# Optimization experiments

Hardware: AMD Instinct MI355X
Metric: run time of the kernel (lower is better)

## Reference

```python
import jax, jax.numpy as jnp
import numpy as np

D_MODEL = 1024
N_STATE = 16
D_INNER = 2 * D_MODEL          # 2048
DT_RANK = (D_MODEL + 15) // 16  # 64 = ceil(d/16)
K_CONV = 4
B, L = 1, 1024


def setup_inputs() -> dict:
    key = jax.random.key(0)
    ks = jax.random.split(key, 9)
    s = lambda fan_in: 1.0 / np.sqrt(fan_in)
    x = jax.random.normal(ks[0], (B, L, D_MODEL), dtype=jnp.float32)
    W_in = jax.random.normal(ks[1], (D_MODEL, 2 * D_INNER), dtype=jnp.float32) * s(D_MODEL)
    conv_w = jax.random.normal(ks[2], (D_INNER, K_CONV), dtype=jnp.float32) * s(K_CONV)
    conv_b = jnp.zeros((D_INNER,), dtype=jnp.float32)
    W_x = jax.random.normal(ks[3], (D_INNER, DT_RANK + 2 * N_STATE), dtype=jnp.float32) * s(D_INNER)
    W_dt = jax.random.normal(ks[4], (DT_RANK, D_INNER), dtype=jnp.float32) * s(DT_RANK)
    b_dt = jax.random.normal(ks[5], (D_INNER,), dtype=jnp.float32) * 0.01
    # A_log initialized as log(1..N) repeated over d_inner, as in __init__
    A_log = jnp.log(jnp.broadcast_to(jnp.arange(1, N_STATE + 1, dtype=jnp.float32), (D_INNER, N_STATE)))
    D = jnp.ones((D_INNER,), dtype=jnp.float32)
    W_out = jax.random.normal(ks[6], (D_INNER, D_MODEL), dtype=jnp.float32) * s(D_INNER)
    return {"x": x, "W_in": W_in, "conv_w": conv_w, "conv_b": conv_b,
            "W_x": W_x, "W_dt": W_dt, "b_dt": b_dt, "A_log": A_log,
            "D": D, "W_out": W_out}


def _causal_dw_conv(x, w, b):
    # x: [B,L,C], w: [C,K], b: [C]; causal depthwise conv (pad left K-1)
    K = w.shape[1]
    xp = jnp.pad(x, ((0, 0), (K - 1, 0), (0, 0)))
    Lx = x.shape[1]
    out = b
    for k in range(K):  # small fixed K=4
        out = out + xp[:, k:k + Lx, :] * w[:, k]
    return out


def _selective_scan(u, delta, A, Bm, Cm, D):
    # u,delta: [B,L,Di]; A: [Di,N]; Bm,Cm: [B,L,N]; D: [Di]
    dA = jnp.exp(delta[..., None] * A)                      # [B,L,Di,N]
    dBu = delta[..., None] * Bm[:, :, None, :] * u[..., None]
    dA_t = jnp.moveaxis(dA, 1, 0)    # [L,B,Di,N]
    dBu_t = jnp.moveaxis(dBu, 1, 0)
    C_t = jnp.moveaxis(Cm, 1, 0)     # [L,B,N]

    def step(h, inp):
        dA_i, dBu_i, C_i = inp
        h = dA_i * h + dBu_i
        y = jnp.einsum('bdn,bn->bd', h, C_i)
        return h, y

    h0 = jnp.zeros(u.shape[:1] + A.shape, dtype=u.dtype)  # [B,Di,N]
    _, ys = jax.lax.scan(step, h0, (dA_t, dBu_t, C_t))
    y = jnp.moveaxis(ys, 0, 1)       # [B,L,Di]
    return y + u * D


def reference(x, W_in, conv_w, conv_b, W_x, W_dt, b_dt, A_log, D, W_out):
    silu = jax.nn.silu
    x_and_res = x @ W_in                                   # [B,L,2*Di]
    x_in, res = jnp.split(x_and_res, 2, axis=-1)
    x_conv = silu(_causal_dw_conv(x_in, conv_w, conv_b))   # [B,L,Di]
    x_dbl = x_conv @ W_x                                   # [B,L,dt_rank+2N]
    dt, Bm, Cm = jnp.split(x_dbl, [DT_RANK, DT_RANK + N_STATE], axis=-1)
    delta = jax.nn.softplus(dt @ W_dt + b_dt)              # [B,L,Di]
    A = -jnp.exp(A_log)                                    # [Di,N]
    y = _selective_scan(x_conv, delta, A, Bm, Cm, D)
    return (y * silu(res)) @ W_out                         # [B,L,d_model]
```

## Files before the change

### kernel.cpp

```cpp
#include <hip/hip_runtime.h>

typedef unsigned short u16;
typedef unsigned int u32;
typedef __attribute__((ext_vector_type(8))) short bf16x8;
typedef __attribute__((ext_vector_type(4))) float f32x4;

#define LSEQ 1024

__device__ __forceinline__ float b2f(u16 v) { return __uint_as_float(((u32)v) << 16); }
__device__ __forceinline__ u16 f2b(float f) {
    u32 x = __float_as_uint(f);
    return (u16)((x + 0x7fffu + ((x >> 16) & 1u)) >> 16);
}
__device__ __forceinline__ float rdf(const void* p, size_t i, int f) {
    return f ? b2f(((const u16*)p)[i]) : ((const float*)p)[i];
}
__device__ __forceinline__ float fsig(float x) {
    return __builtin_amdgcn_rcpf(1.f + __expf(-x));
}

typedef const __attribute__((address_space(1))) u32* gp_t;
typedef __attribute__((address_space(3))) u32* lp_t;
__device__ __forceinline__ void gload16(const u16* g, u16* lds_wave_base) {
    __builtin_amdgcn_global_load_lds((gp_t)g, (lp_t)lds_wave_base, 16, 0, 0);
}

__global__ __launch_bounds__(256) void prep_k(const void* __restrict__ x,
                                              const void* __restrict__ W_in,
                                              const void* __restrict__ W_out,
                                              const void* __restrict__ W_x,
                                              const void* __restrict__ W_dt,
                                              u16* __restrict__ xb,
                                              u16* __restrict__ W_in_t,
                                              u16* __restrict__ W_out_t,
                                              u16* __restrict__ W_x_t,
                                              u16* __restrict__ W_dt_t,
                                              int* __restrict__ flag) {
    __shared__ int cnt;
    __shared__ __align__(8) u16 tile[32][36];
    if (threadIdx.x == 0) cnt = 0;
    __syncthreads();
    const u16* xu = (const u16*)x;
    int c = 0;
#pragma unroll
    for (int j = 0; j < 8; ++j) {
        u16 u = xu[threadIdx.x * 8 + j];
        int e = (u >> 7) & 0xFF;
        c += (e == 0 || (e >= 100 && e <= 140)) ? 1 : 0;
    }
    atomicAdd(&cnt, c);
    __syncthreads();
    const int f = (cnt >= 1638) ? 1 : 0;
    if (blockIdx.x == 0 && threadIdx.x == 0) *flag = f;

    int blk = blockIdx.x;
    if (blk < 1024) {
        int i = (blk * 256 + threadIdx.x) * 4;
        ushort4 o;
        if (f) {
            o = *(const ushort4*)(xu + i);
        } else {
            float4 v = *(const float4*)((const float*)x + i);
            o = make_ushort4(f2b(v.x), f2b(v.y), f2b(v.z), f2b(v.w));
        }
        *(ushort4*)(xb + i) = o;
        return;
    }
    blk -= 1024;
    const void* src; u16* dst; int R, Cn, nbc, t;
    if (blk < 4096)      { src = W_in;  dst = W_in_t;  R = 1024; Cn = 4096; nbc = 128; t = blk; }
    else if (blk < 6144) { src = W_out; dst = W_out_t; R = 2048; Cn = 1024; nbc = 32;  t = blk - 4096; }
    else if (blk < 6400) { src = W_x;   dst = W_x_t;   R = 2048; Cn = 96;   nbc = 4;   t = blk - 6144; }
    else                 { src = W_dt;  dst = W_dt_t;  R = 64;   Cn = 2048; nbc = 64;  t = blk - 6400; }
    int br = t / nbc, bc = t - br * nbc;
    int r0 = br * 32, c0 = bc * 32;
    {
        int ty = threadIdx.x >> 3, tx4 = (threadIdx.x & 7) << 2;
        u16 o0 = 0, o1 = 0, o2 = 0, o3 = 0;
        if (c0 + tx4 < Cn) {
            size_t off = (size_t)(r0 + ty) * Cn + c0 + tx4;
            if (f) {
                ushort4 u = *(const ushort4*)((const u16*)src + off);
                o0 = u.x; o1 = u.y; o2 = u.z; o3 = u.w;
            } else {
                float4 v = *(const float4*)((const float*)src + off);
                o0 = f2b(v.x); o1 = f2b(v.y); o2 = f2b(v.z); o3 = f2b(v.w);
            }
        }
        *(ushort4*)(&tile[ty][tx4]) = make_ushort4(o0, o1, o2, o3);
    }
    __syncthreads();
    {
        int cc = threadIdx.x >> 3, r4 = (threadIdx.x & 7) << 2;
        ushort4 o = make_ushort4(tile[r4][cc], tile[r4 + 1][cc], tile[r4 + 2][cc], tile[r4 + 3][cc]);
        *(ushort4*)(dst + (size_t)(c0 + cc) * R + r0 + r4) = o;
    }
}

template <int MT, int NT, int OUT_MODE>
__global__ __launch_bounds__(256) void gemm_bt(const u16* __restrict__ A,
                                               const u16* __restrict__ Bt,
                                               void* __restrict__ C,
                                               int M, int N, int K,
                                               const int* __restrict__ flag) {
    constexpr int BM = 32 * MT, BN = 32 * NT;
    __shared__ __align__(16) u16 As[2][2 * BM * 32];
    __shared__ __align__(16) u16 Bs[2][2 * BN * 32];
    const int tid = threadIdx.x;
    const int w = tid >> 6, lane = tid & 63;
    const int wm = w & 1, wn = w >> 1;
    const int m_blk = blockIdx.x * BM, n_blk = blockIdx.y * BN;
    const int lm = lane & 15, lq = lane >> 4;
    const int sr = lane >> 2, sc = (lane & 3) << 3;
    const int f = (OUT_MODE == 2) ? flag[0] : 0;

    f32x4 acc[MT][NT];
#pragma unroll
    for (int i = 0; i < MT; ++i)
#pragma unroll
        for (int j = 0; j < NT; ++j) acc[i][j] = (f32x4){0.f, 0.f, 0.f, 0.f};

    auto stage = [&](int buf, int kb) {
#pragma unroll
        for (int cch = 0; cch < 2; ++cch) {
#pragma unroll
            for (int i = 0; i < BM / 64; ++i) {
                int row = i * 64 + w * 16;
                gload16(A + (size_t)(m_blk + row + sr) * K + kb + cch * 32 + sc,
                        &As[buf][cch * BM * 32 + row * 32]);
            }
#pragma unroll
            for (int i = 0; i < BN / 64; ++i) {
                int row = i * 64 + w * 16;
                gload16(Bt + (size_t)(n_blk + row + sr) * K + kb + cch * 32 + sc,
                        &Bs[buf][cch * BN * 32 + row * 32]);
            }
        }
    };
    auto compute = [&](int buf) {
#pragma unroll
        for (int cch = 0; cch < 2; ++cch) {
            bf16x8 af[MT], bf[NT];
#pragma unroll
            for (int tm = 0; tm < MT; ++tm)
                af[tm] = *(const bf16x8*)(&As[buf][cch * BM * 32 +
                                                   (wm * 16 * MT + tm * 16 + lm) * 32 + lq * 8]);
#pragma unroll
            for (int tn = 0; tn < NT; ++tn)
                bf[tn] = *(const bf16x8*)(&Bs[buf][cch * BN * 32 +
                                                   (wn * 16 * NT + tn * 16 + lm) * 32 + lq * 8]);
#pragma unroll
            for (int tm = 0; tm < MT; ++tm)
#pragma unroll
                for (int tn = 0; tn < NT; ++tn)
                    acc[tm][tn] = __builtin_amdgcn_mfma_f32_16x16x32_bf16(af[tm], bf[tn],
                                                                          acc[tm][tn], 0, 0, 0);
        }
    };

    stage(0, 0);
    __syncthreads();
    int cur = 0;
    for (int kb = 64; kb < K; kb += 64) {
        stage(cur ^ 1, kb);
        compute(cur);
        __syncthreads();
        cur ^= 1;
    }
    compute(cur);

#pragma unroll
    for (int tm = 0; tm < MT; ++tm)
#pragma unroll
        for (int tn = 0; tn < NT; ++tn)
#pragma unroll
            for (int r = 0; r < 4; ++r) {
                int row = m_blk + wm * 16 * MT + tm * 16 + lq * 4 + r;
                int col = n_blk + wn * 16 * NT + tn * 16 + lm;
                float v = acc[tm][tn][r];
                if (OUT_MODE == 1) {
                    ((u16*)C)[(size_t)row * N + col] = f2b(v);
                } else {
                    if (f) ((u16*)C)[(size_t)row * N + col] = f2b(v);
                    else   ((float*)C)[(size_t)row * N + col] = v;
                }
            }
}

__global__ __launch_bounds__(256) void gemm2_conv_k(const u16* __restrict__ xz,
                                                    const u16* __restrict__ Bt,
                                                    float* __restrict__ parts,
                                                    u16* __restrict__ xconv,
                                                    const void* __restrict__ cw,
                                                    const void* __restrict__ cb,
                                                    const int* __restrict__ flag) {
    constexpr int MT = 2, NT = 4;
    constexpr int BM = 64, BN = 128, K = 2048, KLEN = 256;
    __shared__ __align__(16) u16 As[2][2 * BM * 32];
    __shared__ __align__(16) u16 Bs[2][2 * BN * 32];
    __shared__ __align__(16) float cws[KLEN * 4];
    __shared__ float cbs[KLEN];
    const int tid = threadIdx.x;
    const int w = tid >> 6, lane = tid & 63;
    const int wm = w & 1, wn = w >> 1;
    const int m_blk = blockIdx.x * BM;
    const int kb0 = blockIdx.z * KLEN;
    const int lm = lane & 15, lq = lane >> 4;
    const int sr = lane >> 2, sc = (lane & 3) << 3;
    const int f = flag[0];

    {
#pragma unroll
        for (int k = 0; k < 4; ++k) cws[tid * 4 + k] = rdf(cw, (size_t)(kb0 + tid) * 4 + k, f);
        cbs[tid] = rdf(cb, kb0 + tid, f);
    }
    __syncthreads();

    f32x4 acc[MT][NT];
#pragma unroll
    for (int i = 0; i < MT; ++i)
#pragma unroll
        for (int j = 0; j < NT; ++j) acc[i][j] = (f32x4){0.f, 0.f, 0.f, 0.f};

    const int arow = tid >> 2;
    const int acg = (tid & 3) << 3;
    const int trow = m_blk + arow;

    auto bstage = [&](int buf, int kb) {
#pragma unroll
        for (int cch = 0; cch < 2; ++cch)
#pragma unroll
            for (int i = 0; i < BN / 64; ++i) {
                int row = i * 64 + w * 16;
                gload16(Bt + (size_t)(row + sr) * K + kb + cch * 32 + sc,
                        &Bs[buf][cch * BN * 32 + row * 32]);
            }
    };
    auto astage = [&](int buf, int cch, int kbase) {
        const int d = kbase + acg;
        const int dl = kbase - kb0 + acg;
        bf16x8 xv[4];
#pragma unroll
        for (int kk = 0; kk < 4; ++kk) {
            bf16x8 zz = {0, 0, 0, 0, 0, 0, 0, 0};
            int tt = trow + kk - 3;
            xv[kk] = (tt >= 0) ? *(const bf16x8*)(xz + (size_t)tt * 4096 + d) : zz;
        }
        bf16x8 rv;
#pragma unroll
        for (int j = 0; j < 8; ++j) {
            f32x4 wv = *(const f32x4*)(cws + (dl + j) * 4);
            float a = cbs[dl + j];
#pragma unroll
            for (int kk = 0; kk < 4; ++kk) a += b2f((u16)xv[kk][j]) * wv[kk];
            rv[j] = (short)f2b(a * fsig(a));
        }
        *(bf16x8*)(&As[buf][cch * BM * 32 + arow * 32 + acg]) = rv;
        *(bf16x8*)(xconv + (size_t)trow * 2048 + d) = rv;
    };
    auto compute = [&](int buf) {
#pragma unroll
        for (int cch = 0; cch < 2; ++cch) {
            bf16x8 af[MT], bf[NT];
#pragma unroll
            for (int tm = 0; tm < MT; ++tm)
                af[tm] = *(const bf16x8*)(&As[buf][cch * BM * 32 +
                                                   (wm * 32 + tm * 16 + lm) * 32 + lq * 8]);
#pragma unroll
            for (int tn = 0; tn < NT; ++tn)
                bf[tn] = *(const bf16x8*)(&Bs[buf][cch * BN * 32 +
                                                   (wn * 64 + tn * 16 + lm) * 32 + lq * 8]);
#pragma unroll
            for (int tm = 0; tm < MT; ++tm)
#pragma unroll
                for (int tn = 0; tn < NT; ++tn)
                    acc[tm][tn] = __builtin_amdgcn_mfma_f32_16x16x32_bf16(af[tm], bf[tn],
                                                                          acc[tm][tn], 0, 0, 0);
        }
    };

    bstage(0, kb0);
    astage(0, 0, kb0);
    astage(0, 1, kb0 + 32);
    __syncthreads();
    int cur = 0;
    for (int kb = kb0 + 64; kb < kb0 + KLEN; kb += 64) {
        bstage(cur ^ 1, kb);
        astage(cur ^ 1, 0, kb);
        astage(cur ^ 1, 1, kb + 32);
        compute(cur);
        __syncthreads();
        cur ^= 1;
    }
    compute(cur);

#pragma unroll
    for (int tm = 0; tm < MT; ++tm)
#pragma unroll
        for (int tn = 0; tn < NT; ++tn)
#pragma unroll
            for (int r = 0; r < 4; ++r) {
                int row = m_blk + wm * 32 + tm * 16 + lq * 4 + r;
                int col = wn * 64 + tn * 16 + lm;
                parts[(size_t)blockIdx.z * 131072 + (size_t)row * 128 + col] = acc[tm][tn][r];
            }
}

__global__ __launch_bounds__(256) void gemm3_red_k(const float* __restrict__ parts,
                                                   const u16* __restrict__ Bt,
                                                   float* __restrict__ delta,
                                                   const void* __restrict__ bias,
                                                   const int* __restrict__ flag) {
    constexpr int MT = 2, NT = 2, BM = 64, BN = 64, K = 64;
    __shared__ __align__(16) u16 As[2 * BM * 32];
    __shared__ __align__(16) u16 Bs[2 * BN * 32];
    const int tid = threadIdx.x;
    const int w = tid >> 6, lane = tid & 63;
    const int wm = w & 1, wn = w >> 1;
    const int m_blk = blockIdx.x * BM, n_blk = blockIdx.y * BN;
    const int lm = lane & 15, lq = lane >> 4;
    const int sr = lane >> 2, sc = (lane & 3) << 3;
    const int f = flag[0];

    f32x4 acc[MT][NT];
#pragma unroll
    for (int i = 0; i < MT; ++i)
#pragma unroll
        for (int j = 0; j < NT; ++j) acc[i][j] = (f32x4){0.f, 0.f, 0.f, 0.f};

    const int arow = tid >> 2;
    const int acg = (tid & 3) << 3;

#pragma unroll
    for (int cch = 0; cch < 2; ++cch) {
        int row = w * 16;
        gload16(Bt + (size_t)(n_blk + row + sr) * K + cch * 32 + sc, &Bs[cch * BN * 32 + row * 32]);
    }
#pragma unroll
    for (int cch = 0; cch < 2; ++cch) {
        f32x4 s0 = {0.f, 0.f, 0.f, 0.f}, s1 = {0.f, 0.f, 0.f, 0.f};
#pragma unroll
        for (int sl = 0; sl < 8; ++sl) {
            const float* p = parts + (size_t)sl * 131072 + (size_t)(m_blk + arow) * 128 + cch * 32 + acg;
            s0 += *(const f32x4*)p;
            s1 += *(const f32x4*)(p + 4);
        }
        bf16x8 rv;
#pragma unroll
        for (int j = 0; j < 4; ++j) {
            rv[j] = (short)f2b(s0[j]);
            rv[4 + j] = (short)f2b(s1[j]);
        }
        *(bf16x8*)(&As[cch * BM * 32 + arow * 32 + acg]) = rv;
    }
    __syncthreads();

#pragma unroll
    for (int cch = 0; cch < 2; ++cch) {
        bf16x8 af[MT], bf[NT];
#pragma unroll
        for (int tm = 0; tm < MT; ++tm)
            af[tm] = *(const bf16x8*)(&As[cch * BM * 32 + (wm * 32 + tm * 16 + lm) * 32 + lq * 8]);
#pragma unroll
        for (int tn = 0; tn < NT; ++tn)
            bf[tn] = *(const bf16x8*)(&Bs[cch * BN * 32 + (wn * 32 + tn * 16 + lm) * 32 + lq * 8]);
#pragma unroll
        for (int tm = 0; tm < MT; ++tm)
#pragma unroll
            for (int tn = 0; tn < NT; ++tn)
                acc[tm][tn] = __builtin_amdgcn_mfma_f32_16x16x32_bf16(af[tm], bf[tn],
                                                                      acc[tm][tn], 0, 0, 0);
    }

#pragma unroll
    for (int tm = 0; tm < MT; ++tm)
#pragma unroll
        for (int tn = 0; tn < NT; ++tn)
#pragma unroll
            for (int r = 0; r < 4; ++r) {
                int row = m_blk + wm * 32 + tm * 16 + lq * 4 + r;
                int col = n_blk + wn * 32 + tn * 16 + lm;
                float b = rdf(bias, col, f);
                float t2 = acc[tm][tn][r] + b;
                float sp = fmaxf(t2, 0.f) + __logf(1.f + __expf(-fabsf(t2)));
                delta[(size_t)row * 2048 + col] = sp;
            }
}

__global__ __launch_bounds__(256) void scan1_k(const float* __restrict__ delta,
                                               const u16* __restrict__ xc,
                                               const float* __restrict__ parts,
                                               const void* __restrict__ A_log,
                                               float* __restrict__ Acar,
                                               float* __restrict__ Bcar,
                                               const int* __restrict__ flag) {
    __shared__ float BCs[32][32];
    const int f = *flag;
    const int g = blockIdx.x * 256 + threadIdx.x;
    const int c = g >> 12, rem = g & 4095;
    const int d = rem >> 1, nh = rem & 1;
    const int n0 = nh << 3;
    const int t0 = c * 32;
    {
        int idx = threadIdx.x * 4;
        int tl = idx >> 5, col = idx & 31;
        f32x4 s = {0.f, 0.f, 0.f, 0.f};
#pragma unroll
        for (int sl = 0; sl < 8; ++sl)
            s += *(const f32x4*)(parts + (size_t)sl * 131072 + (size_t)(t0 + tl) * 128 + 64 + col);
        *(f32x4*)&BCs[tl][col] = s;
    }
    __syncthreads();

    float A[8], P[8], h[8];
#pragma unroll
    for (int j = 0; j < 8; ++j) {
        A[j] = -__expf(rdf(A_log, d * 16 + n0 + j, f));
        P[j] = 1.f;
        h[j] = 0.f;
    }
#pragma unroll 4
    for (int i = 0; i < 32; ++i) {
        int t = t0 + i;
        float de = delta[t * 2048 + d];
        float dBu = de * b2f(xc[t * 2048 + d]);
        f32x4 Bv0 = *(const f32x4*)&BCs[i][n0];
        f32x4 Bv1 = *(const f32x4*)&BCs[i][n0 + 4];
#pragma unroll
        for (int j = 0; j < 8; ++j) {
            float Bv = (j < 4) ? Bv0[j & 3] : Bv1[j & 3];
            float a = __expf(de * A[j]);
            h[j] = a * h[j] + Bv * dBu;
            P[j] *= a;
        }
    }
    f32x4 pa0 = {P[0], P[1], P[2], P[3]}, pa1 = {P[4], P[5], P[6], P[7]};
    f32x4 hb0 = {h[0], h[1], h[2], h[3]}, hb1 = {h[4], h[5], h[6], h[7]};
    size_t base = (size_t)c * 32768 + d * 16 + n0;
    *(f32x4*)(Acar + base) = pa0;
    *(f32x4*)(Acar + base + 4) = pa1;
    *(f32x4*)(Bcar + base) = hb0;
    *(f32x4*)(Bcar + base + 4) = hb1;
}

__global__ __launch_bounds__(64) void scan2_k(const float* __restrict__ Acar,
                                              float* __restrict__ Bcar) {
    int idx = blockIdx.x * 64 + threadIdx.x;
    float a[32], b[32];
#pragma unroll
    for (int c = 0; c < 32; ++c) {
        a[c] = Acar[c * 32768 + idx];
        b[c] = Bcar[c * 32768 + idx];
    }
    float H = 0.f;
#pragma unroll
    for (int c = 0; c < 32; ++c) {
        float t = b[c];
        b[c] = H;
        H = a[c] * H + t;
    }
#pragma unroll
    for (int c = 0; c < 32; ++c) Bcar[c * 32768 + idx] = b[c];
}

__global__ __launch_bounds__(256) void scan3_k(const float* __restrict__ delta,
                                               const u16* __restrict__ xc,
                                               const float* __restrict__ parts,
                                               const u16* __restrict__ xz,
                                               const void* __restrict__ A_log,
                                               const void* __restrict__ Dvp,
                                               const float* __restrict__ Bcar,
                                               u16* __restrict__ yg,
                                               const int* __restrict__ flag) {
    __shared__ float BCs[32][32];
    const int f = *flag;
    const int g = blockIdx.x * 256 + threadIdx.x;
    const int c = g >> 12, rem = g & 4095;
    const int d = rem >> 1, nh = rem & 1;
    const int n0 = nh << 3;
    const int t0 = c * 32;
    {
        int idx = threadIdx.x * 4;
        int tl = idx >> 5, col = idx & 31;
        f32x4 s = {0.f, 0.f, 0.f, 0.f};
#pragma unroll
        for (int sl = 0; sl < 8; ++sl)
            s += *(const f32x4*)(parts + (size_t)sl * 131072 + (size_t)(t0 + tl) * 128 + 64 + col);
        *(f32x4*)&BCs[tl][col] = s;
    }
    __syncthreads();

    float A[8], h[8];
    size_t base = (size_t)c * 32768 + d * 16 + n0;
    f32x4 h0 = *(const f32x4*)(Bcar + base);
    f32x4 h1 = *(const f32x4*)(Bcar + base + 4);
#pragma unroll
    for (int j = 0; j < 8; ++j) {
        A[j] = -__expf(rdf(A_log, d * 16 + n0 + j, f));
        h[j] = (j < 4) ? h0[j & 3] : h1[j & 3];
    }
    float Dd = rdf(Dvp, d, f);
#pragma unroll 4
    for (int i = 0; i < 32; ++i) {
        int t = t0 + i;
        float de = delta[t * 2048 + d];
        float u = b2f(xc[t * 2048 + d]);
        float dBu = de * u;
        f32x4 Bv0 = *(const f32x4*)&BCs[i][n0];
        f32x4 Bv1 = *(const f32x4*)&BCs[i][n0 + 4];
        f32x4 Cv0 = *(const f32x4*)&BCs[i][16 + n0];
        f32x4 Cv1 = *(const f32x4*)&BCs[i][20 + n0];
        float p = 0.f;
#pragma unroll
        for (int j = 0; j < 8; ++j) {
            float Bv = (j < 4) ? Bv0[j & 3] : Bv1[j & 3];
            float Cv = (j < 4) ? Cv0[j & 3] : Cv1[j & 3];
            float a = __expf(de * A[j]);
            h[j] = a * h[j] + Bv * dBu;
            p += h[j] * Cv;
        }
        p += __shfl_xor(p, 1);
        if (nh == 0) {
            float r = b2f(xz[(size_t)t * 4096 + 2048 + d]);
            float yt = p + u * Dd;
            yg[t * 2048 + d] = f2b(yt * r * fsig(r));
        }
    }
}

__global__ __launch_bounds__(256) void scan_k(const float* __restrict__ delta,
                                              const u16* __restrict__ xc,
                                              const float* __restrict__ parts,
                                              const u16* __restrict__ xz,
                                              const void* __restrict__ A_log,
                                              const void* __restrict__ Dvp,
                                              u16* __restrict__ yg,
                                              const int* __restrict__ flag) {
    int f = *flag;
    int g = blockIdx.x * 256 + threadIdx.x;
    int d = g >> 4, n = g & 15;
    float A = -__expf(rdf(A_log, d * 16 + n, f));
    float Dd = rdf(Dvp, d, f);
    float h = 0.f;
    for (int t = 0; t < LSEQ; ++t) {
        float de = delta[t * 2048 + d];
        float u = b2f(xc[t * 2048 + d]);
        float Bv = 0.f, Cv = 0.f;
#pragma unroll
        for (int sl = 0; sl < 8; ++sl) {
            Bv += parts[(size_t)sl * 131072 + (size_t)t * 128 + 64 + n];
            Cv += parts[(size_t)sl * 131072 + (size_t)t * 128 + 80 + n];
        }
        h = __expf(de * A) * h + (de * Bv) * u;
        float p = h * Cv;
        p += __shfl_xor(p, 1);
        p += __shfl_xor(p, 2);
        p += __shfl_xor(p, 4);
        p += __shfl_xor(p, 8);
        if (n == 0) {
            float r = b2f(xz[(size_t)t * 4096 + 2048 + d]);
            float yt = p + u * Dd;
            yg[t * 2048 + d] = f2b(yt * r * fsig(r));
        }
    }
}

extern "C" void kernel_launch(void* const* d_in, const int* in_sizes, int n_in,
                              void* d_out, int out_size, void* d_ws, size_t ws_size,
                              hipStream_t stream) {
    const void* x      = d_in[0];
    const void* W_in   = d_in[1];
    const void* conv_w = d_in[2];
    const void* conv_b = d_in[3];
    const void* W_x    = d_in[4];
    const void* W_dt   = d_in[5];
    const void* b_dt   = d_in[6];
    const void* A_log  = d_in[7];
    const void* Dv     = d_in[8];
    const void* W_out  = d_in[9];

    char* ws = (char*)d_ws;
    u16*   xz     = (u16*)(ws);
    u16*   xconv  = (u16*)(ws + 8388608);
    float* parts  = (float*)(ws + 12582912);
    float* delta  = (float*)(ws + 17432576);
    u16*   W_in_t = (u16*)(ws + 17432576);
    u16*   yg     = (u16*)(ws + 25821184);
    u16*   xb     = (u16*)(ws + 25821184);
    u16*   W_x_t  = (u16*)(ws + 30015488);
    u16*   W_dt_t = (u16*)(ws + 30539776);
    u16*   W_out_t= (u16*)(ws + 30801920);
    int*   flag   = (int*)(ws + 34996224);
    float* Acar   = (float*)(ws + 34996352);
    float* Bcar   = (float*)(ws + 39190656);
    const bool chunked_ok = (ws_size >= 43384960);

    prep_k<<<7552, 256, 0, stream>>>(x, W_in, W_out, W_x, W_dt,
                                     xb, W_in_t, W_out_t, W_x_t, W_dt_t, flag);
    gemm_bt<2, 4, 1><<<dim3(16, 32), 256, 0, stream>>>(xb, W_in_t, (void*)xz,
                                                       1024, 4096, 1024, flag);
    gemm2_conv_k<<<dim3(16, 1, 8), 256, 0, stream>>>(xz, W_x_t, parts, xconv,
                                                     conv_w, conv_b, flag);
    gemm3_red_k<<<dim3(16, 32), 256, 0, stream>>>(parts, W_dt_t, delta, b_dt, flag);

    if (chunked_ok) {
        scan1_k<<<512, 256, 0, stream>>>(delta, xconv, parts, A_log, Acar, Bcar, flag);
        scan2_k<<<512, 64, 0, stream>>>(Acar, Bcar);
        scan3_k<<<512, 256, 0, stream>>>(delta, xconv, parts, xz, A_log, Dv, Bcar, yg, flag);
    } else {
        scan_k<<<128, 256, 0, stream>>>(delta, xconv, parts, xz, A_log, Dv, yg, flag);
    }

    gemm_bt<2, 2, 2><<<dim3(16, 16), 256, 0, stream>>>(yg, W_out_t, d_out,
                                                       1024, 1024, 2048, flag);
}
```

Baseline: 217.1 us.

## Fuse delta projection GEMM and softplus into chunked scan kernels

Removes the separate gemm3_red_k launch and the 8 MB fp32 delta buffer on the chunked path. Each scan1/scan3 block now reduces the dt slice of the split-K partials, runs a small MFMA GEMM against W_dt, and applies softplus into an LDS tile for its 32x128 chunk. This trades a global write and two reads of delta for computing the delta tile twice, once in each scan pass, plus extra LDS use per block. The workspace layout is compacted, and the fallback path reuses the Acar region for delta.

```diff
diff --git a/kernel.cpp b/kernel.cpp
--- a/kernel.cpp
+++ b/kernel.cpp
@@ -6,6 +6,7 @@
 typedef __attribute__((ext_vector_type(4))) float f32x4;
 
 #define LSEQ 1024
+#define NSL 8
 
 __device__ __forceinline__ float b2f(u16 v) { return __uint_as_float(((u32)v) << 16); }
 __device__ __forceinline__ u16 f2b(float f) {
@@ -306,6 +307,232 @@
             }
 }
 
+__device__ __forceinline__ void delta_tile(const float* __restrict__ parts,
+                                           const u16* __restrict__ Wdt,
+                                           const void* __restrict__ bias,
+                                           int f, int t0, int d0,
+                                           u16* As2, u16* Bs2, float (*dlt)[128],
+                                           int tid, int w, int lm, int lq, int sr, int sc) {
+#pragma unroll
+    for (int cch = 0; cch < 2; ++cch)
+#pragma unroll
+        for (int i = 0; i < 2; ++i) {
+            int row = i * 64 + w * 16;
+            gload16(Wdt + (size_t)(d0 + row + sr) * 64 + cch * 32 + sc,
+                    Bs2 + cch * 4096 + row * 32);
+        }
+    {
+        int arow = tid >> 3, acg = (tid & 7) << 3;
+        f32x4 s0 = {0.f, 0.f, 0.f, 0.f}, s1 = {0.f, 0.f, 0.f, 0.f};
+#pragma unroll
+        for (int sl = 0; sl < NSL; ++sl) {
+            const float* p = parts + (size_t)sl * 131072 + (size_t)(t0 + arow) * 128 + acg;
+            s0 += *(const f32x4*)p;
+            s1 += *(const f32x4*)(p + 4);
+        }
+        bf16x8 rv;
+#pragma unroll
+        for (int j = 0; j < 4; ++j) {
+            rv[j] = (short)f2b(s0[j]);
+            rv[4 + j] = (short)f2b(s1[j]);
+        }
+        *(bf16x8*)(As2 + (acg >> 5) * 1024 + arow * 32 + (acg & 31)) = rv;
+    }
+    __syncthreads();
+
+    f32x4 dacc[2][2];
+#pragma unroll
+    for (int i = 0; i < 2; ++i)
+#pragma unroll
+        for (int j = 0; j < 2; ++j) dacc[i][j] = (f32x4){0.f, 0.f, 0.f, 0.f};
+#pragma unroll
+    for (int cch = 0; cch < 2; ++cch) {
+        bf16x8 af[2], bf[2];
+#pragma unroll
+        for (int tm = 0; tm < 2; ++tm)
+            af[tm] = *(const bf16x8*)(As2 + cch * 1024 + (tm * 16 + lm) * 32 + lq * 8);
+#pragma unroll
+        for (int tn = 0; tn < 2; ++tn)
+            bf[tn] = *(const bf16x8*)(Bs2 + cch * 4096 + (w * 32 + tn * 16 + lm) * 32 + lq * 8);
+#pragma unroll
+        for (int tm = 0; tm < 2; ++tm)
+#pragma unroll
+            for (int tn = 0; tn < 2; ++tn)
+                dacc[tm][tn] = __builtin_amdgcn_mfma_f32_16x16x32_bf16(af[tm], bf[tn],
+                                                                       dacc[tm][tn], 0, 0, 0);
+    }
+#pragma unroll
+    for (int tm = 0; tm < 2; ++tm)
+#pragma unroll
+        for (int tn = 0; tn < 2; ++tn)
+#pragma unroll
+            for (int r = 0; r < 4; ++r) {
+                int row = tm * 16 + lq * 4 + r;
+                int col = w * 32 + tn * 16 + lm;
+                float b = rdf(bias, d0 + col, f);
+                float t2 = dacc[tm][tn][r] + b;
+                dlt[row][col] = fmaxf(t2, 0.f) + __logf(1.f + __expf(-fabsf(t2)));
+            }
+    __syncthreads();
+}
+
+__global__ __launch_bounds__(256) void scan1_k(const u16* __restrict__ xc,
+                                               const float* __restrict__ parts,
+                                               const u16* __restrict__ Wdt,
+                                               const void* __restrict__ bias,
+                                               const void* __restrict__ A_log,
+                                               float* __restrict__ Acar,
+                                               float* __restrict__ Bcar,
+                                               const int* __restrict__ flag) {
+    __shared__ __align__(16) u16 As2[2 * 32 * 32];
+    __shared__ __align__(16) u16 Bs2[2 * 128 * 32];
+    __shared__ float dlt[32][128];
+    __shared__ float BCs[32][32];
+    const int f = *flag;
+    const int tid = threadIdx.x, b = blockIdx.x;
+    const int w = tid >> 6, lane = tid & 63;
+    const int lm = lane & 15, lq = lane >> 4;
+    const int sr = lane >> 2, sc = (lane & 3) << 3;
+    const int c = b >> 4;
+    const int d0 = (b & 15) * 128;
+    const int t0 = c * 32;
+    {
+        int idx = tid * 4;
+        int tl = idx >> 5, col = idx & 31;
+        f32x4 s = {0.f, 0.f, 0.f, 0.f};
+#pragma unroll
+        for (int sl = 0; sl < NSL; ++sl)
+            s += *(const f32x4*)(parts + (size_t)sl * 131072 + (size_t)(t0 + tl) * 128 + 64 + col);
+        *(f32x4*)&BCs[tl][col] = s;
+    }
+    delta_tile(parts, Wdt, bias, f, t0, d0, As2, Bs2, dlt, tid, w, lm, lq, sr, sc);
+
+    const int dl = tid >> 1, nh = tid & 1;
+    const int d = d0 + dl, n0 = nh << 3;
+    float A[8], P[8], h[8];
+#pragma unroll
+    for (int j = 0; j < 8; ++j) {
+        A[j] = -__expf(rdf(A_log, d * 16 + n0 + j, f));
+        P[j] = 1.f;
+        h[j] = 0.f;
+    }
+#pragma unroll 4
+    for (int i = 0; i < 32; ++i) {
+        int t = t0 + i;
+        float de = dlt[i][dl];
+        float dBu = de * b2f(xc[t * 2048 + d]);
+        f32x4 Bv0 = *(const f32x4*)&BCs[i][n0];
+        f32x4 Bv1 = *(const f32x4*)&BCs[i][n0 + 4];
+#pragma unroll
+        for (int j = 0; j < 8; ++j) {
+            float Bv = (j < 4) ? Bv0[j & 3] : Bv1[j & 3];
+            float a = __expf(de * A[j]);
+            h[j] = a * h[j] + Bv * dBu;
+            P[j] *= a;
+        }
+    }
+    f32x4 pa0 = {P[0], P[1], P[2], P[3]}, pa1 = {P[4], P[5], P[6], P[7]};
+    f32x4 hb0 = {h[0], h[1], h[2], h[3]}, hb1 = {h[4], h[5], h[6], h[7]};
+    size_t base = (size_t)c * 32768 + d * 16 + n0;
+    *(f32x4*)(Acar + base) = pa0;
+    *(f32x4*)(Acar + base + 4) = pa1;
+    *(f32x4*)(Bcar + base) = hb0;
+    *(f32x4*)(Bcar + base + 4) = hb1;
+}
+
+__global__ __launch_bounds__(64) void scan2_k(const float* __restrict__ Acar,
+                                              float* __restrict__ Bcar) {
+    int idx = blockIdx.x * 64 + threadIdx.x;
+    float a[32], b[32];
+#pragma unroll
+    for (int c = 0; c < 32; ++c) {
+        a[c] = Acar[c * 32768 + idx];
+        b[c] = Bcar[c * 32768 + idx];
+    }
+    float H = 0.f;
+#pragma unroll
+    for (int c = 0; c < 32; ++c) {
+        float t = b[c];
+        b[c] = H;
+        H = a[c] * H + t;
+    }
+#pragma unroll
+    for (int c = 0; c < 32; ++c) Bcar[c * 32768 + idx] = b[c];
+}
+
+__global__ __launch_bounds__(256) void scan3_k(const u16* __restrict__ xc,
+                                               const float* __restrict__ parts,
+                                               const u16* __restrict__ Wdt,
+                                               const void* __restrict__ bias,
+                                               const u16* __restrict__ xz,
+                                               const void* __restrict__ A_log,
+                                               const void* __restrict__ Dvp,
+                                               const float* __restrict__ Bcar,
+                                               u16* __restrict__ yg,
+                                               const int* __restrict__ flag) {
+    __shared__ __align__(16) u16 As2[2 * 32 * 32];
+    __shared__ __align__(16) u16 Bs2[2 * 128 * 32];
+    __shared__ float dlt[32][128];
+    __shared__ float BCs[32][32];
+    const int f = *flag;
+    const int tid = threadIdx.x, b = blockIdx.x;
+    const int w = tid >> 6, lane = tid & 63;
+    const int lm = lane & 15, lq = lane >> 4;
+    const int sr = lane >> 2, sc = (lane & 3) << 3;
+    const int c = b >> 4;
+    const int d0 = (b & 15) * 128;
+    const int t0 = c * 32;
+    {
+        int idx = tid * 4;
+        int tl = idx >> 5, col = idx & 31;
+        f32x4 s = {0.f, 0.f, 0.f, 0.f};
+#pragma unroll
+        for (int sl = 0; sl < NSL; ++sl)
+            s += *(const f32x4*)(parts + (size_t)sl * 131072 + (size_t)(t0 + tl) * 128 + 64 + col);
+        *(f32x4*)&BCs[tl][col] = s;
+    }
+    delta_tile(parts, Wdt, bias, f, t0, d0, As2, Bs2, dlt, tid, w, lm, lq, sr, sc);
+
+    const int dl = tid >> 1, nh = tid & 1;
+    const int d = d0 + dl, n0 = nh << 3;
+    float A[8], h[8];
+    size_t base = (size_t)c * 32768 + d * 16 + n0;
+    f32x4 h0 = *(const f32x4*)(Bcar + base);
+    f32x4 h1 = *(const f32x4*)(Bcar + base + 4);
+#pragma unroll
+    for (int j = 0; j < 8; ++j) {
+        A[j] = -__expf(rdf(A_log, d * 16 + n0 + j, f));
+        h[j] = (j < 4) ? h0[j & 3] : h1[j & 3];
+    }
+    float Dd = rdf(Dvp, d, f);
+#pragma unroll 4
+    for (int i = 0; i < 32; ++i) {
+        int t = t0 + i;
+        float de = dlt[i][dl];
+        float u = b2f(xc[t * 2048 + d]);
+        float dBu = de * u;
+        f32x4 Bv0 = *(const f32x4*)&BCs[i][n0];
+        f32x4 Bv1 = *(const f32x4*)&BCs[i][n0 + 4];
+        f32x4 Cv0 = *(const f32x4*)&BCs[i][16 + n0];
+        f32x4 Cv1 = *(const f32x4*)&BCs[i][20 + n0];
+        float p = 0.f;
+#pragma unroll
+        for (int j = 0; j < 8; ++j) {
+            float Bv = (j < 4) ? Bv0[j & 3] : Bv1[j & 3];
+            float Cv = (j < 4) ? Cv0[j & 3] : Cv1[j & 3];
+            float a = __expf(de * A[j]);
+            h[j] = a * h[j] + Bv * dBu;
+            p += h[j] * Cv;
+        }
+        p += __shfl_xor(p, 1);
+        if (nh == 0) {
+            float r = b2f(xz[(size_t)t * 4096 + 2048 + d]);
+            float yt = p + u * Dd;
+            yg[t * 2048 + d] = f2b(yt * r * fsig(r));
+        }
+    }
+}
+
 __global__ __launch_bounds__(256) void gemm3_red_k(const float* __restrict__ parts,
                                                    const u16* __restrict__ Bt,
                                                    float* __restrict__ delta,
@@ -340,7 +567,7 @@
     for (int cch = 0; cch < 2; ++cch) {
         f32x4 s0 = {0.f, 0.f, 0.f, 0.f}, s1 = {0.f, 0.f, 0.f, 0.f};
 #pragma unroll
-        for (int sl = 0; sl < 8; ++sl) {
+        for (int sl = 0; sl < NSL; ++sl) {
             const float* p = parts + (size_t)sl * 131072 + (size_t)(m_blk + arow) * 128 + cch * 32 + acg;
             s0 += *(const f32x4*)p;
             s1 += *(const f32x4*)(p + 4);
@@ -385,147 +612,6 @@
                 float sp = fmaxf(t2, 0.f) + __logf(1.f + __expf(-fabsf(t2)));
                 delta[(size_t)row * 2048 + col] = sp;
             }
-}
-
-__global__ __launch_bounds__(256) void scan1_k(const float* __restrict__ delta,
-                                               const u16* __restrict__ xc,
-                                               const float* __restrict__ parts,
-                                               const void* __restrict__ A_log,
-                                               float* __restrict__ Acar,
-                                               float* __restrict__ Bcar,
-                                               const int* __restrict__ flag) {
-    __shared__ float BCs[32][32];
-    const int f = *flag;
-    const int g = blockIdx.x * 256 + threadIdx.x;
-    const int c = g >> 12, rem = g & 4095;
-    const int d = rem >> 1, nh = rem & 1;
-    const int n0 = nh << 3;
-    const int t0 = c * 32;
-    {
-        int idx = threadIdx.x * 4;
-        int tl = idx >> 5, col = idx & 31;
-        f32x4 s = {0.f, 0.f, 0.f, 0.f};
-#pragma unroll
-        for (int sl = 0; sl < 8; ++sl)
-            s += *(const f32x4*)(parts + (size_t)sl * 131072 + (size_t)(t0 + tl) * 128 + 64 + col);
-        *(f32x4*)&BCs[tl][col] = s;
-    }
-    __syncthreads();
-
-    float A[8], P[8], h[8];
-#pragma unroll
-    for (int j = 0; j < 8; ++j) {
-        A[j] = -__expf(rdf(A_log, d * 16 + n0 + j, f));
-        P[j] = 1.f;
-        h[j] = 0.f;
-    }
-#pragma unroll 4
-    for (int i = 0; i < 32; ++i) {
-        int t = t0 + i;
-        float de = delta[t * 2048 + d];
-        float dBu = de * b2f(xc[t * 2048 + d]);
-        f32x4 Bv0 = *(const f32x4*)&BCs[i][n0];
-        f32x4 Bv1 = *(const f32x4*)&BCs[i][n0 + 4];
-#pragma unroll
-        for (int j = 0; j < 8; ++j) {
-            float Bv = (j < 4) ? Bv0[j & 3] : Bv1[j & 3];
-            float a = __expf(de * A[j]);
-            h[j] = a * h[j] + Bv * dBu;
-            P[j] *= a;
-        }
-    }
-    f32x4 pa0 = {P[0], P[1], P[2], P[3]}, pa1 = {P[4], P[5], P[6], P[7]};
-    f32x4 hb0 = {h[0], h[1], h[2], h[3]}, hb1 = {h[4], h[5], h[6], h[7]};
-    size_t base = (size_t)c * 32768 + d * 16 + n0;
-    *(f32x4*)(Acar + base) = pa0;
-    *(f32x4*)(Acar + base + 4) = pa1;
-    *(f32x4*)(Bcar + base) = hb0;
-    *(f32x4*)(Bcar + base + 4) = hb1;
-}
-
-__global__ __launch_bounds__(64) void scan2_k(const float* __restrict__ Acar,
-                                              float* __restrict__ Bcar) {
-    int idx = blockIdx.x * 64 + threadIdx.x;
-    float a[32], b[32];
-#pragma unroll
-    for (int c = 0; c < 32; ++c) {
-        a[c] = Acar[c * 32768 + idx];
-        b[c] = Bcar[c * 32768 + idx];
-    }
-    float H = 0.f;
-#pragma unroll
-    for (int c = 0; c < 32; ++c) {
-        float t = b[c];
-        b[c] = H;
-        H = a[c] * H + t;
-    }
-#pragma unroll
-    for (int c = 0; c < 32; ++c) Bcar[c * 32768 + idx] = b[c];
-}
-
-__global__ __launch_bounds__(256) void scan3_k(const float* __restrict__ delta,
-                                               const u16* __restrict__ xc,
-                                               const float* __restrict__ parts,
-                                               const u16* __restrict__ xz,
-                                               const void* __restrict__ A_log,
-                                               const void* __restrict__ Dvp,
-                                               const float* __restrict__ Bcar,
-                                               u16* __restrict__ yg,
-                                               const int* __restrict__ flag) {
-    __shared__ float BCs[32][32];
-    const int f = *flag;
-    const int g = blockIdx.x * 256 + threadIdx.x;
-    const int c = g >> 12, rem = g & 4095;
-    const int d = rem >> 1, nh = rem & 1;
-    const int n0 = nh << 3;
-    const int t0 = c * 32;
-    {
-        int idx = threadIdx.x * 4;
-        int tl = idx >> 5, col = idx & 31;
-        f32x4 s = {0.f, 0.f, 0.f, 0.f};
-#pragma unroll
-        for (int sl = 0; sl < 8; ++sl)
-            s += *(const f32x4*)(parts + (size_t)sl * 131072 + (size_t)(t0 + tl) * 128 + 64 + col);
-        *(f32x4*)&BCs[tl][col] = s;
-    }
-    __syncthreads();
-
-    float A[8], h[8];
-    size_t base = (size_t)c * 32768 + d * 16 + n0;
-    f32x4 h0 = *(const f32x4*)(Bcar + base);
-    f32x4 h1 = *(const f32x4*)(Bcar + base + 4);
-#pragma unroll
-    for (int j = 0; j < 8; ++j) {
-        A[j] = -__expf(rdf(A_log, d * 16 + n0 + j, f));
-        h[j] = (j < 4) ? h0[j & 3] : h1[j & 3];
-    }
-    float Dd = rdf(Dvp, d, f);
-#pragma unroll 4
-    for (int i = 0; i < 32; ++i) {
-        int t = t0 + i;
-        float de = delta[t * 2048 + d];
-        float u = b2f(xc[t * 2048 + d]);
-        float dBu = de * u;
-        f32x4 Bv0 = *(const f32x4*)&BCs[i][n0];
-        f32x4 Bv1 = *(const f32x4*)&BCs[i][n0 + 4];
-        f32x4 Cv0 = *(const f32x4*)&BCs[i][16 + n0];
-        f32x4 Cv1 = *(const f32x4*)&BCs[i][20 + n0];
-        float p = 0.f;
-#pragma unroll
-        for (int j = 0; j < 8; ++j) {
-            float Bv = (j < 4) ? Bv0[j & 3] : Bv1[j & 3];
-            float Cv = (j < 4) ? Cv0[j & 3] : Cv1[j & 3];
-            float a = __expf(de * A[j]);
-            h[j] = a * h[j] + Bv * dBu;
-            p += h[j] * Cv;
-        }
-        p += __shfl_xor(p, 1);
-        if (nh == 0) {
-            float r = b2f(xz[(size_t)t * 4096 + 2048 + d]);
-            float yt = p + u * Dd;
-            yg[t * 2048 + d] = f2b(yt * r * fsig(r));
-        }
-    }
 }
 
 __global__ __launch_bounds__(256) void scan_k(const float* __restrict__ delta,
@@ -547,7 +633,7 @@
         float u = b2f(xc[t * 2048 + d]);
         float Bv = 0.f, Cv = 0.f;
 #pragma unroll
-        for (int sl = 0; sl < 8; ++sl) {
+        for (int sl = 0; sl < NSL; ++sl) {
             Bv += parts[(size_t)sl * 131072 + (size_t)t * 128 + 64 + n];
             Cv += parts[(size_t)sl * 131072 + (size_t)t * 128 + 80 + n];
         }
@@ -583,17 +669,17 @@
     u16*   xz     = (u16*)(ws);
     u16*   xconv  = (u16*)(ws + 8388608);
     float* parts  = (float*)(ws + 12582912);
-    float* delta  = (float*)(ws + 17432576);
-    u16*   W_in_t = (u16*)(ws + 17432576);
-    u16*   yg     = (u16*)(ws + 25821184);
-    u16*   xb     = (u16*)(ws + 25821184);
-    u16*   W_x_t  = (u16*)(ws + 30015488);
-    u16*   W_dt_t = (u16*)(ws + 30539776);
-    u16*   W_out_t= (u16*)(ws + 30801920);
-    int*   flag   = (int*)(ws + 34996224);
-    float* Acar   = (float*)(ws + 34996352);
-    float* Bcar   = (float*)(ws + 39190656);
-    const bool chunked_ok = (ws_size >= 43384960);
+    u16*   W_in_t = (u16*)(ws + 16777216);
+    u16*   yg     = (u16*)(ws + 25165824);
+    u16*   xb     = (u16*)(ws + 25165824);
+    u16*   W_x_t  = (u16*)(ws + 29360128);
+    u16*   W_dt_t = (u16*)(ws + 29884416);
+    u16*   W_out_t= (u16*)(ws + 30146560);
+    int*   flag   = (int*)(ws + 34340864);
+    float* Acar   = (float*)(ws + 34340992);
+    float* Bcar   = (float*)(ws + 38535296);
+    float* dfb    = (float*)(ws + 34340992);
+    const bool chunked_ok = (ws_size >= 42729600);
 
     prep_k<<<7552, 256, 0, stream>>>(x, W_in, W_out, W_x, W_dt,
                                      xb, W_in_t, W_out_t, W_x_t, W_dt_t, flag);
@@ -601,14 +687,15 @@
                                                        1024, 4096, 1024, flag);
     gemm2_conv_k<<<dim3(16, 1, 8), 256, 0, stream>>>(xz, W_x_t, parts, xconv,
                                                      conv_w, conv_b, flag);
-    gemm3_red_k<<<dim3(16, 32), 256, 0, stream>>>(parts, W_dt_t, delta, b_dt, flag);
 
     if (chunked_ok) {
-        scan1_k<<<512, 256, 0, stream>>>(delta, xconv, parts, A_log, Acar, Bcar, flag);
+        scan1_k<<<512, 256, 0, stream>>>(xconv, parts, W_dt_t, b_dt, A_log, Acar, Bcar, flag);
         scan2_k<<<512, 64, 0, stream>>>(Acar, Bcar);
-        scan3_k<<<512, 256, 0, stream>>>(delta, xconv, parts, xz, A_log, Dv, Bcar, yg, flag);
+        scan3_k<<<512, 256, 0, stream>>>(xconv, parts, W_dt_t, b_dt, xz, A_log, Dv,
+                                         Bcar, yg, flag);
     } else {
-        scan_k<<<128, 256, 0, stream>>>(delta, xconv, parts, xz, A_log, Dv, yg, flag);
+        gemm3_red_k<<<dim3(16, 32), 256, 0, stream>>>(parts, W_dt_t, dfb, b_dt, flag);
+        scan_k<<<128, 256, 0, stream>>>(dfb, xconv, parts, xz, A_log, Dv, yg, flag);
     }
 
     gemm_bt<2, 2, 2><<<dim3(16, 16), 256, 0, stream>>>(yg, W_out_t, d_out,
```

New measurement: 210.6 us. 1.03x faster.
